# Optimization experiments

Measured on AMD Instinct MI355X. Metric: run time of the kernel, lower is better.

Reference implementation:

```python
import jax, jax.numpy as jnp
import numpy as np

LEAKY_ALPHA = 0.2

def setup_inputs() -> dict:
    key = jax.random.key(0)
    kA, kH, kW, k1, k2 = jax.random.split(key, 5)
    B, N, F_in, D = 8, 2048, 256, 128
    return {
        "A": jax.random.normal(kA, (B, N, N), dtype=jnp.float32),
        "H": jax.random.normal(kH, (B, N, F_in), dtype=jnp.float32),
        "W": jax.random.normal(kW, (F_in, D), dtype=jnp.float32) * 0.05,
        "a_1": jax.random.normal(k1, (D, 1), dtype=jnp.float32) * 0.05,
        "a_2": jax.random.normal(k2, (D, 1), dtype=jnp.float32) * 0.05,
    }

def reference(A, H, W, a_1, a_2):
    # H_: [B, N, D] node projections
    H_ = jnp.einsum('bnf,fd->bnd', H, W)
    # additive attention logits: f1[b,i] + f2[b,j] -> [B, N, N]
    f1 = H_ @ a_1            # [B, N, 1]
    f2 = H_ @ a_2            # [B, N, 1]
    e = jax.nn.leaky_relu(f1 + jnp.swapaxes(f2, 1, 2), negative_slope=LEAKY_ALPHA)
    # NOTE: original multiplies logits by the binary adjacency (not -inf masking)
    mask = (A > 0.0).astype(jnp.float32)
    alpha = jax.nn.softmax(e * mask, axis=-1)   # [B, N, N]
    H_next = jnp.matmul(alpha, H_)              # [B, N, D]
    return H_next
```

## Files before the change

kernel.cpp:

```cpp
#include <hip/hip_runtime.h>


#define LEAKY 0.2f
constexpr int Bb = 8, Nn = 2048, FIN = 256, Dd = 128;
constexpr int NROW = Bb * Nn;

typedef __attribute__((ext_vector_type(8))) short short8;
typedef __attribute__((ext_vector_type(4))) float float4v;

__device__ __forceinline__ unsigned short f2bf(float f) {
    union { float f; unsigned int i; } v; v.f = f;
    return (unsigned short)((v.i + 0x8000u) >> 16);
}

__global__ __launch_bounds__(256) void prep_wt(const float* __restrict__ W,
                                               unsigned short* __restrict__ Wt) {
    int idx = blockIdx.x * 256 + threadIdx.x;
    int k = idx >> 7, d = idx & 127;
    Wt[d * FIN + k] = f2bf(W[idx]);
}

__global__ __launch_bounds__(256) void proj_kernel(
    const float* __restrict__ Hg,
    const unsigned short* __restrict__ Wt,
    const float* __restrict__ a1, const float* __restrict__ a2,
    unsigned short* __restrict__ Hbt,
    float* __restrict__ f1g, float* __restrict__ f2g) {
    constexpr int WS = 264;
    __shared__ unsigned short Wl[128 * WS];
    __shared__ float Fb[2][2][2][16];
    const int tid = threadIdx.x;

    #pragma unroll
    for (int p = 0; p < 16; ++p) {
        int i8 = p * 2048 + tid * 8;
        int n = i8 >> 8, k = i8 & 255;
        *(uint4*)(Wl + n * WS + k) = *(const uint4*)(Wt + i8);
    }
    __syncthreads();

    const int wave = tid >> 6, lane = tid & 63;
    const int r = wave >> 1, h = wave & 1;
    const int q = lane >> 4, m = lane & 15;
    const int row0 = blockIdx.x * 32 + 16 * r;
    const float* hrow = Hg + (size_t)(row0 + m) * FIN;

    float4v acc[4] = {};
    #pragma unroll 2
    for (int c = 0; c < 8; ++c) {
        float4 ha = *(const float4*)(hrow + 32 * c + 8 * q);
        float4 hb = *(const float4*)(hrow + 32 * c + 8 * q + 4);
        union { short8 v; unsigned int u[4]; } A;
        A.u[0] = (unsigned)f2bf(ha.x) | ((unsigned)f2bf(ha.y) << 16);
        A.u[1] = (unsigned)f2bf(ha.z) | ((unsigned)f2bf(ha.w) << 16);
        A.u[2] = (unsigned)f2bf(hb.x) | ((unsigned)f2bf(hb.y) << 16);
        A.u[3] = (unsigned)f2bf(hb.z) | ((unsigned)f2bf(hb.w) << 16);
        #pragma unroll
        for (int t = 0; t < 4; ++t) {
            int n = 64 * h + 16 * t + m;
            short8 bfr = *(const short8*)(Wl + n * WS + 32 * c + 8 * q);
            acc[t] = __builtin_amdgcn_mfma_f32_16x16x32_bf16(A.v, bfr, acc[t], 0, 0, 0);
        }
    }
    float p1[4] = {0.f, 0.f, 0.f, 0.f}, p2[4] = {0.f, 0.f, 0.f, 0.f};
    #pragma unroll
    for (int t = 0; t < 4; ++t) {
        int n = 64 * h + 16 * t + m;
        ushort4 hv;
        hv.x = f2bf(acc[t][0]); hv.y = f2bf(acc[t][1]);
        hv.z = f2bf(acc[t][2]); hv.w = f2bf(acc[t][3]);
        *(ushort4*)(Hbt + (size_t)n * NROW + row0 + 4 * q) = hv;
        float w1 = a1[n], w2 = a2[n];
        #pragma unroll
        for (int rg = 0; rg < 4; ++rg) {
            p1[rg] = fmaf(acc[t][rg], w1, p1[rg]);
            p2[rg] = fmaf(acc[t][rg], w2, p2[rg]);
        }
    }
    #pragma unroll
    for (int off = 1; off <= 8; off <<= 1) {
        #pragma unroll
        for (int rg = 0; rg < 4; ++rg) {
            p1[rg] += __shfl_xor(p1[rg], off, 64);
            p2[rg] += __shfl_xor(p2[rg], off, 64);
        }
    }
    if (m == 0) {
        #pragma unroll
        for (int rg = 0; rg < 4; ++rg) {
            Fb[0][r][h][4 * q + rg] = p1[rg];
            Fb[1][r][h][4 * q + rg] = p2[rg];
        }
    }
    __syncthreads();
    if (tid < 32) {
        int r2 = tid >> 4, i = tid & 15;
        int row = blockIdx.x * 32 + 16 * r2 + i;
        f1g[row] = Fb[0][r2][0][i] + Fb[0][r2][1][i];
        f2g[row] = Fb[1][r2][0][i] + Fb[1][r2][1][i];
    }
}

__global__ __launch_bounds__(256) void attn_kernel(
    const float* __restrict__ Ag,
    const unsigned short* __restrict__ Hbt,
    const float* __restrict__ f1g, const float* __restrict__ f2g,
    float* __restrict__ Og) {
    constexpr int RS = 132;
    __shared__ float Rbuf[4 * 16 * RS];
    __shared__ float Lbuf[4][16];

    const int tid = threadIdx.x;
    const int w = tid >> 6, lane = tid & 63;
    const int q = lane >> 4, m = lane & 15;
    const int b = blockIdx.y;
    const int i0 = blockIdx.x * 16;
    const size_t bRow = (size_t)b * Nn;

    const float fi = f1g[bRow + i0 + m];
    const float* Arow = Ag + (bRow + i0 + m) * (size_t)Nn;
    const float* f2p = f2g + bRow;
    const unsigned short* Bbase = Hbt + (size_t)m * NROW + bRow;

    float4v acc[8] = {};
    float lsum = 0.f;
    const int j0 = w * (Nn / 4);

    #pragma unroll 2
    for (int jt = j0; jt < j0 + Nn / 4; jt += 64) {
        short8 pa[2];
        #pragma unroll
        for (int c = 0; c < 2; ++c) {
            int col = jt + 32 * c + 8 * q;
            float4 a0 = *(const float4*)(Arow + col);
            float4 a1v = *(const float4*)(Arow + col + 4);
            float4 fa = *(const float4*)(f2p + col);
            float4 fb = *(const float4*)(f2p + col + 4);
            float av[8] = {a0.x, a0.y, a0.z, a0.w, a1v.x, a1v.y, a1v.z, a1v.w};
            float fv[8] = {fa.x, fa.y, fa.z, fa.w, fb.x, fb.y, fb.z, fb.w};
            union { short8 v; unsigned short us[8]; } P;
            #pragma unroll
            for (int j = 0; j < 8; ++j) {
                float s = fi + fv[j];
                float e = fmaxf(s, LEAKY * s);
                e = fminf(e, 30.f);
                float p = (av[j] > 0.f) ? __expf(e) : 1.0f;
                P.us[j] = f2bf(p);
                lsum += p;
            }
            pa[c] = P.v;
        }
        #pragma unroll
        for (int t = 0; t < 8; ++t) {
            const unsigned short* bp = Bbase + (size_t)(16 * t) * NROW + jt + 8 * q;
            short8 b0 = *(const short8*)(bp);
            short8 b1 = *(const short8*)(bp + 32);
            acc[t] = __builtin_amdgcn_mfma_f32_16x16x32_bf16(pa[0], b0, acc[t], 0, 0, 0);
            acc[t] = __builtin_amdgcn_mfma_f32_16x16x32_bf16(pa[1], b1, acc[t], 0, 0, 0);
        }
    }

    lsum += __shfl_xor(lsum, 16, 64);
    lsum += __shfl_xor(lsum, 32, 64);
    if (lane < 16) Lbuf[w][lane] = lsum;
    #pragma unroll
    for (int t = 0; t < 8; ++t)
        #pragma unroll
        for (int rg = 0; rg < 4; ++rg)
            Rbuf[w * 16 * RS + (4 * q + rg) * RS + 16 * t + m] = acc[t][rg];
    __syncthreads();

    const int row = tid >> 4, c4 = tid & 15;
    float l = Lbuf[0][row] + Lbuf[1][row] + Lbuf[2][row] + Lbuf[3][row];
    float rl = 1.0f / l;
    float* orow = Og + (bRow + i0 + row) * (size_t)Dd;
    #pragma unroll
    for (int half = 0; half < 2; ++half) {
        int col = 64 * half + 4 * c4;
        const float* rb = Rbuf + row * RS + col;
        float4 s0 = *(const float4*)(rb);
        float4 s1 = *(const float4*)(rb + 16 * RS);
        float4 s2 = *(const float4*)(rb + 32 * RS);
        float4 s3 = *(const float4*)(rb + 48 * RS);
        float4 o;
        o.x = (s0.x + s1.x + s2.x + s3.x) * rl;
        o.y = (s0.y + s1.y + s2.y + s3.y) * rl;
        o.z = (s0.z + s1.z + s2.z + s3.z) * rl;
        o.w = (s0.w + s1.w + s2.w + s3.w) * rl;
        *(float4*)(orow + col) = o;
    }
}

extern "C" void kernel_launch(void* const* d_in, const int* in_sizes, int n_in,
                              void* d_out, int out_size, void* d_ws, size_t ws_size,
                              hipStream_t stream) {
    const float* A  = (const float*)d_in[0];
    const float* H  = (const float*)d_in[1];
    const float* W  = (const float*)d_in[2];
    const float* a1 = (const float*)d_in[3];
    const float* a2 = (const float*)d_in[4];
    float* out = (float*)d_out;

    unsigned short* Wt  = (unsigned short*)d_ws;
    unsigned short* Hbt = Wt + FIN * Dd;
    float* f1 = (float*)(Hbt + (size_t)Dd * NROW);
    float* f2 = f1 + NROW;

    prep_wt<<<dim3(FIN * Dd / 256), 256, 0, stream>>>(W, Wt);
    proj_kernel<<<dim3(NROW / 32), 256, 0, stream>>>(H, Wt, a1, a2, Hbt, f1, f2);
    attn_kernel<<<dim3(Nn / 16, Bb), 256, 0, stream>>>(A, Hbt, f1, f2, out);
}
```

Measured before the change: 259.8 us.

## Software-pipeline A/f2 loads in attention and drop LDS staging in projection

```diff
diff --git a/kernel.cpp b/kernel.cpp
--- a/kernel.cpp
+++ b/kernel.cpp
@@ -20,52 +20,48 @@
     Wt[d * FIN + k] = f2bf(W[idx]);
 }
 
-__global__ __launch_bounds__(256) void proj_kernel(
+__global__ __launch_bounds__(128) void proj_kernel(
     const float* __restrict__ Hg,
     const unsigned short* __restrict__ Wt,
     const float* __restrict__ a1, const float* __restrict__ a2,
     unsigned short* __restrict__ Hbt,
     float* __restrict__ f1g, float* __restrict__ f2g) {
-    constexpr int WS = 264;
-    __shared__ unsigned short Wl[128 * WS];
-    __shared__ float Fb[2][2][2][16];
     const int tid = threadIdx.x;
-
-    #pragma unroll
-    for (int p = 0; p < 16; ++p) {
-        int i8 = p * 2048 + tid * 8;
-        int n = i8 >> 8, k = i8 & 255;
-        *(uint4*)(Wl + n * WS + k) = *(const uint4*)(Wt + i8);
-    }
-    __syncthreads();
-
     const int wave = tid >> 6, lane = tid & 63;
-    const int r = wave >> 1, h = wave & 1;
     const int q = lane >> 4, m = lane & 15;
-    const int row0 = blockIdx.x * 32 + 16 * r;
+    const int row0 = blockIdx.x * 32 + 16 * wave;
     const float* hrow = Hg + (size_t)(row0 + m) * FIN;
 
-    float4v acc[4] = {};
-    #pragma unroll 2
+    float4v acc[8] = {};
+    float4 Ab0 = *(const float4*)(hrow + 8 * q);
+    float4 Ab1 = *(const float4*)(hrow + 8 * q + 4);
+
+    #pragma unroll
     for (int c = 0; c < 8; ++c) {
-        float4 ha = *(const float4*)(hrow + 32 * c + 8 * q);
-        float4 hb = *(const float4*)(hrow + 32 * c + 8 * q + 4);
         union { short8 v; unsigned int u[4]; } A;
-        A.u[0] = (unsigned)f2bf(ha.x) | ((unsigned)f2bf(ha.y) << 16);
-        A.u[1] = (unsigned)f2bf(ha.z) | ((unsigned)f2bf(ha.w) << 16);
-        A.u[2] = (unsigned)f2bf(hb.x) | ((unsigned)f2bf(hb.y) << 16);
-        A.u[3] = (unsigned)f2bf(hb.z) | ((unsigned)f2bf(hb.w) << 16);
-        #pragma unroll
-        for (int t = 0; t < 4; ++t) {
-            int n = 64 * h + 16 * t + m;
-            short8 bfr = *(const short8*)(Wl + n * WS + 32 * c + 8 * q);
-            acc[t] = __builtin_amdgcn_mfma_f32_16x16x32_bf16(A.v, bfr, acc[t], 0, 0, 0);
-        }
-    }
+        A.u[0] = (unsigned)f2bf(Ab0.x) | ((unsigned)f2bf(Ab0.y) << 16);
+        A.u[1] = (unsigned)f2bf(Ab0.z) | ((unsigned)f2bf(Ab0.w) << 16);
+        A.u[2] = (unsigned)f2bf(Ab1.x) | ((unsigned)f2bf(Ab1.y) << 16);
+        A.u[3] = (unsigned)f2bf(Ab1.z) | ((unsigned)f2bf(Ab1.w) << 16);
+        short8 bf[8];
+        #pragma unroll
+        for (int t = 0; t < 8; ++t)
+            bf[t] = *(const short8*)(Wt + (size_t)(16 * t + m) * FIN + 32 * c + 8 * q);
+        __builtin_amdgcn_sched_barrier(0);
+        if (c < 7) {
+            Ab0 = *(const float4*)(hrow + 32 * (c + 1) + 8 * q);
+            Ab1 = *(const float4*)(hrow + 32 * (c + 1) + 8 * q + 4);
+        }
+        __builtin_amdgcn_sched_barrier(0);
+        #pragma unroll
+        for (int t = 0; t < 8; ++t)
+            acc[t] = __builtin_amdgcn_mfma_f32_16x16x32_bf16(A.v, bf[t], acc[t], 0, 0, 0);
+    }
+
     float p1[4] = {0.f, 0.f, 0.f, 0.f}, p2[4] = {0.f, 0.f, 0.f, 0.f};
     #pragma unroll
-    for (int t = 0; t < 4; ++t) {
-        int n = 64 * h + 16 * t + m;
+    for (int t = 0; t < 8; ++t) {
+        int n = 16 * t + m;
         ushort4 hv;
         hv.x = f2bf(acc[t][0]); hv.y = f2bf(acc[t][1]);
         hv.z = f2bf(acc[t][2]); hv.w = f2bf(acc[t][3]);
@@ -88,16 +84,9 @@
     if (m == 0) {
         #pragma unroll
         for (int rg = 0; rg < 4; ++rg) {
-            Fb[0][r][h][4 * q + rg] = p1[rg];
-            Fb[1][r][h][4 * q + rg] = p2[rg];
-        }
-    }
-    __syncthreads();
-    if (tid < 32) {
-        int r2 = tid >> 4, i = tid & 15;
-        int row = blockIdx.x * 32 + 16 * r2 + i;
-        f1g[row] = Fb[0][r2][0][i] + Fb[0][r2][1][i];
-        f2g[row] = Fb[1][r2][0][i] + Fb[1][r2][1][i];
+            f1g[row0 + 4 * q + rg] = p1[rg];
+            f2g[row0 + 4 * q + rg] = p2[rg];
+        }
     }
 }
 
@@ -125,19 +114,26 @@
     float4v acc[8] = {};
     float lsum = 0.f;
     const int j0 = w * (Nn / 4);
-
-    #pragma unroll 2
-    for (int jt = j0; jt < j0 + Nn / 4; jt += 64) {
+    const int jend = j0 + Nn / 4;
+
+    float4 Ab[4], Fb[4];
+    Ab[0] = *(const float4*)(Arow + j0 + 8 * q);
+    Ab[1] = *(const float4*)(Arow + j0 + 8 * q + 4);
+    Ab[2] = *(const float4*)(Arow + j0 + 32 + 8 * q);
+    Ab[3] = *(const float4*)(Arow + j0 + 32 + 8 * q + 4);
+    Fb[0] = *(const float4*)(f2p + j0 + 8 * q);
+    Fb[1] = *(const float4*)(f2p + j0 + 8 * q + 4);
+    Fb[2] = *(const float4*)(f2p + j0 + 32 + 8 * q);
+    Fb[3] = *(const float4*)(f2p + j0 + 32 + 8 * q + 4);
+
+    for (int jt = j0; jt < jend; jt += 64) {
         short8 pa[2];
         #pragma unroll
         for (int c = 0; c < 2; ++c) {
-            int col = jt + 32 * c + 8 * q;
-            float4 a0 = *(const float4*)(Arow + col);
-            float4 a1v = *(const float4*)(Arow + col + 4);
-            float4 fa = *(const float4*)(f2p + col);
-            float4 fb = *(const float4*)(f2p + col + 4);
-            float av[8] = {a0.x, a0.y, a0.z, a0.w, a1v.x, a1v.y, a1v.z, a1v.w};
-            float fv[8] = {fa.x, fa.y, fa.z, fa.w, fb.x, fb.y, fb.z, fb.w};
+            float av[8] = {Ab[2*c].x, Ab[2*c].y, Ab[2*c].z, Ab[2*c].w,
+                           Ab[2*c+1].x, Ab[2*c+1].y, Ab[2*c+1].z, Ab[2*c+1].w};
+            float fv[8] = {Fb[2*c].x, Fb[2*c].y, Fb[2*c].z, Fb[2*c].w,
+                           Fb[2*c+1].x, Fb[2*c+1].y, Fb[2*c+1].z, Fb[2*c+1].w};
             union { short8 v; unsigned short us[8]; } P;
             #pragma unroll
             for (int j = 0; j < 8; ++j) {
@@ -150,13 +146,31 @@
             }
             pa[c] = P.v;
         }
+        short8 bf[16];
         #pragma unroll
         for (int t = 0; t < 8; ++t) {
             const unsigned short* bp = Bbase + (size_t)(16 * t) * NROW + jt + 8 * q;
-            short8 b0 = *(const short8*)(bp);
-            short8 b1 = *(const short8*)(bp + 32);
-            acc[t] = __builtin_amdgcn_mfma_f32_16x16x32_bf16(pa[0], b0, acc[t], 0, 0, 0);
-            acc[t] = __builtin_amdgcn_mfma_f32_16x16x32_bf16(pa[1], b1, acc[t], 0, 0, 0);
+            bf[2 * t]     = *(const short8*)(bp);
+            bf[2 * t + 1] = *(const short8*)(bp + 32);
+        }
+        __builtin_amdgcn_sched_barrier(0);
+        if (jt + 64 < jend) {
+            const float* ar = Arow + jt + 64;
+            Ab[0] = *(const float4*)(ar + 8 * q);
+            Ab[1] = *(const float4*)(ar + 8 * q + 4);
+            Ab[2] = *(const float4*)(ar + 32 + 8 * q);
+            Ab[3] = *(const float4*)(ar + 32 + 8 * q + 4);
+            const float* fr = f2p + jt + 64;
+            Fb[0] = *(const float4*)(fr + 8 * q);
+            Fb[1] = *(const float4*)(fr + 8 * q + 4);
+            Fb[2] = *(const float4*)(fr + 32 + 8 * q);
+            Fb[3] = *(const float4*)(fr + 32 + 8 * q + 4);
+        }
+        __builtin_amdgcn_sched_barrier(0);
+        #pragma unroll
+        for (int t = 0; t < 8; ++t) {
+            acc[t] = __builtin_amdgcn_mfma_f32_16x16x32_bf16(pa[0], bf[2*t],     acc[t], 0, 0, 0);
+            acc[t] = __builtin_amdgcn_mfma_f32_16x16x32_bf16(pa[1], bf[2*t + 1], acc[t], 0, 0, 0);
         }
     }
 
@@ -207,6 +221,6 @@
     float* f2 = f1 + NROW;
 
     prep_wt<<<dim3(FIN * Dd / 256), 256, 0, stream>>>(W, Wt);
-    proj_kernel<<<dim3(NROW / 32), 256, 0, stream>>>(H, Wt, a1, a2, Hbt, f1, f2);
+    proj_kernel<<<dim3(NROW / 32), 128, 0, stream>>>(H, Wt, a1, a2, Hbt, f1, f2);
     attn_kernel<<<dim3(Nn / 16, Bb), 256, 0, stream>>>(A, Hbt, f1, f2, out);
 }
```

New measurement: 253.7 us. -2.3%, faster.

## Stage A tiles through double-buffered LDS and pack H and W in MFMA fragment layout

Applied to the files above, without the earlier changes.

```diff
diff --git a/kernel.cpp b/kernel.cpp
--- a/kernel.cpp
+++ b/kernel.cpp
@@ -4,6 +4,7 @@
 #define LEAKY 0.2f
 constexpr int Bb = 8, Nn = 2048, FIN = 256, Dd = 128;
 constexpr int NROW = Bb * Nn;
+constexpr int RS = 132;
 
 typedef __attribute__((ext_vector_type(8))) short short8;
 typedef __attribute__((ext_vector_type(4))) float float4v;
@@ -13,138 +14,173 @@
     return (unsigned short)((v.i + 0x8000u) >> 16);
 }
 
-__global__ __launch_bounds__(256) void prep_wt(const float* __restrict__ W,
-                                               unsigned short* __restrict__ Wt) {
+__device__ __forceinline__ void stage_read(const float* __restrict__ base, int rstride,
+                                           int tid, float4* st) {
+    const int row = tid >> 4, c16 = tid & 15;
+    const float* p = base + (size_t)row * rstride + c16 * 4;
+    #pragma unroll
+    for (int k = 0; k < 4; ++k) st[k] = *(const float4*)(p + 64 * k);
+}
+__device__ __forceinline__ void stage_write(float* __restrict__ As, int tid, const float4* st) {
+    const int row = tid >> 4, c16 = tid & 15, sw = row & 7;
+    float* dst = As + row * 256;
+    #pragma unroll
+    for (int k = 0; k < 4; ++k) {
+        const int col = 4 * (c16 + 16 * k);
+        dst[(col + 0) ^ sw] = st[k].x;
+        dst[(col + 1) ^ sw] = st[k].y;
+        dst[(col + 2) ^ sw] = st[k].z;
+        dst[(col + 3) ^ sw] = st[k].w;
+    }
+}
+
+__global__ __launch_bounds__(256) void prep_wf(const float* __restrict__ W,
+                                               unsigned short* __restrict__ Wf) {
     int idx = blockIdx.x * 256 + threadIdx.x;
     int k = idx >> 7, d = idx & 127;
-    Wt[d * FIN + k] = f2bf(W[idx]);
+    Wf[(size_t)((k >> 3) * 128 + d) * 8 + (k & 7)] = f2bf(W[idx]);
 }
 
 __global__ __launch_bounds__(256) void proj_kernel(
     const float* __restrict__ Hg,
-    const unsigned short* __restrict__ Wt,
+    const unsigned short* __restrict__ Wf,
     const float* __restrict__ a1, const float* __restrict__ a2,
-    unsigned short* __restrict__ Hbt,
+    unsigned short* __restrict__ Hbt2,
     float* __restrict__ f1g, float* __restrict__ f2g) {
-    constexpr int WS = 264;
-    __shared__ unsigned short Wl[128 * WS];
-    __shared__ float Fb[2][2][2][16];
+    __shared__ float Rbuf[4 * 16 * RS];
+    __shared__ float Hs[4096];
+
     const int tid = threadIdx.x;
-
-    #pragma unroll
-    for (int p = 0; p < 16; ++p) {
-        int i8 = p * 2048 + tid * 8;
-        int n = i8 >> 8, k = i8 & 255;
-        *(uint4*)(Wl + n * WS + k) = *(const uint4*)(Wt + i8);
-    }
-    __syncthreads();
-
-    const int wave = tid >> 6, lane = tid & 63;
-    const int r = wave >> 1, h = wave & 1;
-    const int q = lane >> 4, m = lane & 15;
-    const int row0 = blockIdx.x * 32 + 16 * r;
-    const float* hrow = Hg + (size_t)(row0 + m) * FIN;
-
-    float4v acc[4] = {};
-    #pragma unroll 2
-    for (int c = 0; c < 8; ++c) {
-        float4 ha = *(const float4*)(hrow + 32 * c + 8 * q);
-        float4 hb = *(const float4*)(hrow + 32 * c + 8 * q + 4);
-        union { short8 v; unsigned int u[4]; } A;
-        A.u[0] = (unsigned)f2bf(ha.x) | ((unsigned)f2bf(ha.y) << 16);
-        A.u[1] = (unsigned)f2bf(ha.z) | ((unsigned)f2bf(ha.w) << 16);
-        A.u[2] = (unsigned)f2bf(hb.x) | ((unsigned)f2bf(hb.y) << 16);
-        A.u[3] = (unsigned)f2bf(hb.z) | ((unsigned)f2bf(hb.w) << 16);
-        #pragma unroll
-        for (int t = 0; t < 4; ++t) {
-            int n = 64 * h + 16 * t + m;
-            short8 bfr = *(const short8*)(Wl + n * WS + 32 * c + 8 * q);
-            acc[t] = __builtin_amdgcn_mfma_f32_16x16x32_bf16(A.v, bfr, acc[t], 0, 0, 0);
-        }
-    }
-    float p1[4] = {0.f, 0.f, 0.f, 0.f}, p2[4] = {0.f, 0.f, 0.f, 0.f};
-    #pragma unroll
-    for (int t = 0; t < 4; ++t) {
-        int n = 64 * h + 16 * t + m;
-        ushort4 hv;
-        hv.x = f2bf(acc[t][0]); hv.y = f2bf(acc[t][1]);
-        hv.z = f2bf(acc[t][2]); hv.w = f2bf(acc[t][3]);
-        *(ushort4*)(Hbt + (size_t)n * NROW + row0 + 4 * q) = hv;
-        float w1 = a1[n], w2 = a2[n];
-        #pragma unroll
-        for (int rg = 0; rg < 4; ++rg) {
-            p1[rg] = fmaf(acc[t][rg], w1, p1[rg]);
-            p2[rg] = fmaf(acc[t][rg], w2, p2[rg]);
-        }
-    }
-    #pragma unroll
-    for (int off = 1; off <= 8; off <<= 1) {
-        #pragma unroll
-        for (int rg = 0; rg < 4; ++rg) {
-            p1[rg] += __shfl_xor(p1[rg], off, 64);
-            p2[rg] += __shfl_xor(p2[rg], off, 64);
-        }
-    }
-    if (m == 0) {
-        #pragma unroll
-        for (int rg = 0; rg < 4; ++rg) {
-            Fb[0][r][h][4 * q + rg] = p1[rg];
-            Fb[1][r][h][4 * q + rg] = p2[rg];
-        }
-    }
-    __syncthreads();
-    if (tid < 32) {
-        int r2 = tid >> 4, i = tid & 15;
-        int row = blockIdx.x * 32 + 16 * r2 + i;
-        f1g[row] = Fb[0][r2][0][i] + Fb[0][r2][1][i];
-        f2g[row] = Fb[1][r2][0][i] + Fb[1][r2][1][i];
-    }
+    const int w = tid >> 6, lane = tid & 63, q = lane >> 4, m = lane & 15;
+    const int row0 = blockIdx.x * 16;
+
+    float4 st[4];
+    stage_read(Hg + (size_t)row0 * FIN, FIN, tid, st);
+    stage_write(Hs, tid, st);
+    __syncthreads();
+
+    float4v acc[8] = {};
+    const float* arow = Hs + m * 256;
+    const int sw = m & 7;
+    #pragma unroll
+    for (int c = 0; c < 2; ++c) {
+        const int cb = w * 64 + 32 * c + 8 * q;
+        union { short8 v; unsigned short us[8]; } Af;
+        #pragma unroll
+        for (int j = 0; j < 8; ++j) Af.us[j] = f2bf(arow[cb + (j ^ sw)]);
+        #pragma unroll
+        for (int t = 0; t < 8; ++t) {
+            const short8 bfr = *(const short8*)(Wf + (size_t)((8 * w + 4 * c + q) * 128 + 16 * t + m) * 8);
+            acc[t] = __builtin_amdgcn_mfma_f32_16x16x32_bf16(Af.v, bfr, acc[t], 0, 0, 0);
+        }
+    }
+    #pragma unroll
+    for (int t = 0; t < 8; ++t)
+        #pragma unroll
+        for (int rg = 0; rg < 4; ++rg)
+            Rbuf[w * 16 * RS + (4 * q + rg) * RS + 16 * t + m] = acc[t][rg];
+    __syncthreads();
+
+    const int row = tid >> 4, c4 = tid & 15;
+    float o[8];
+    #pragma unroll
+    for (int half = 0; half < 2; ++half) {
+        const int col = 64 * half + 4 * c4;
+        const float* rb = Rbuf + row * RS + col;
+        float4 s0 = *(const float4*)(rb);
+        float4 s1 = *(const float4*)(rb + 16 * RS);
+        float4 s2 = *(const float4*)(rb + 32 * RS);
+        float4 s3 = *(const float4*)(rb + 48 * RS);
+        o[4 * half + 0] = s0.x + s1.x + s2.x + s3.x;
+        o[4 * half + 1] = s0.y + s1.y + s2.y + s3.y;
+        o[4 * half + 2] = s0.z + s1.z + s2.z + s3.z;
+        o[4 * half + 3] = s0.w + s1.w + s2.w + s3.w;
+    }
+    {
+        float4 A1a = *(const float4*)(a1 + 4 * c4), A1b = *(const float4*)(a1 + 64 + 4 * c4);
+        float4 A2a = *(const float4*)(a2 + 4 * c4), A2b = *(const float4*)(a2 + 64 + 4 * c4);
+        float p1 = o[0]*A1a.x + o[1]*A1a.y + o[2]*A1a.z + o[3]*A1a.w
+                 + o[4]*A1b.x + o[5]*A1b.y + o[6]*A1b.z + o[7]*A1b.w;
+        float p2 = o[0]*A2a.x + o[1]*A2a.y + o[2]*A2a.z + o[3]*A2a.w
+                 + o[4]*A2b.x + o[5]*A2b.y + o[6]*A2b.z + o[7]*A2b.w;
+        #pragma unroll
+        for (int off = 1; off <= 8; off <<= 1) {
+            p1 += __shfl_xor(p1, off, 16);
+            p2 += __shfl_xor(p2, off, 16);
+        }
+        if (c4 == 0) { f1g[row0 + row] = p1; f2g[row0 + row] = p2; }
+    }
+    *(float4*)(Rbuf + row * RS + 4 * c4)      = make_float4(o[0], o[1], o[2], o[3]);
+    *(float4*)(Rbuf + row * RS + 64 + 4 * c4) = make_float4(o[4], o[5], o[6], o[7]);
+    __syncthreads();
+    const int d = tid >> 1, h = tid & 1;
+    union { uint4 v; unsigned short us[8]; } oP;
+    #pragma unroll
+    for (int r = 0; r < 8; ++r) oP.us[r] = f2bf(Rbuf[(8 * h + r) * RS + d]);
+    *(uint4*)(Hbt2 + (size_t)((2 * blockIdx.x + h) * 128 + d) * 8) = oP.v;
 }
 
 __global__ __launch_bounds__(256) void attn_kernel(
     const float* __restrict__ Ag,
-    const unsigned short* __restrict__ Hbt,
+    const unsigned short* __restrict__ Hbt2,
     const float* __restrict__ f1g, const float* __restrict__ f2g,
     float* __restrict__ Og) {
-    constexpr int RS = 132;
-    __shared__ float Rbuf[4 * 16 * RS];
+    __shared__ float smem[8448];
+    __shared__ float f2s[2][256];
     __shared__ float Lbuf[4][16];
 
     const int tid = threadIdx.x;
-    const int w = tid >> 6, lane = tid & 63;
-    const int q = lane >> 4, m = lane & 15;
-    const int b = blockIdx.y;
-    const int i0 = blockIdx.x * 16;
+    const int w = tid >> 6, lane = tid & 63, q = lane >> 4, m = lane & 15;
+    const int b = blockIdx.y, i0 = blockIdx.x * 16;
     const size_t bRow = (size_t)b * Nn;
 
     const float fi = f1g[bRow + i0 + m];
-    const float* Arow = Ag + (bRow + i0 + m) * (size_t)Nn;
+    const float* Abase = Ag + (bRow + i0) * (size_t)Nn;
     const float* f2p = f2g + bRow;
-    const unsigned short* Bbase = Hbt + (size_t)m * NROW + bRow;
+    const unsigned short* Bb2 = Hbt2 + bRow * 128;
+    const int jw = w * 64;
 
     float4v acc[8] = {};
     float lsum = 0.f;
-    const int j0 = w * (Nn / 4);
-
-    #pragma unroll 2
-    for (int jt = j0; jt < j0 + Nn / 4; jt += 64) {
+    float4 st[4], fst;
+
+    stage_read(Abase, Nn, tid, st);
+    if (tid < 64) fst = *(const float4*)(f2p + tid * 4);
+    stage_write(smem, tid, st);
+    if (tid < 64) *(float4*)(&f2s[0][tid * 4]) = fst;
+
+    for (int ch = 0; ch < 8; ++ch) {
+        __syncthreads();
+        const int jt = ch * 256;
+        const float* As = smem + (ch & 1) * 4096;
+        const float* f2c = &f2s[ch & 1][0];
+        const unsigned short* bg = Bb2 + (size_t)((jt + jw) >> 3) * 1024;
+        short8 bf[16];
+        #pragma unroll
+        for (int t = 0; t < 8; ++t) {
+            bf[2 * t]     = *(const short8*)(bg + ((size_t)(q    ) * 128 + 16 * t + m) * 8);
+            bf[2 * t + 1] = *(const short8*)(bg + ((size_t)(q + 4) * 128 + 16 * t + m) * 8);
+        }
+        __builtin_amdgcn_sched_barrier(0);
+        if (ch < 7) {
+            stage_read(Abase + jt + 256, Nn, tid, st);
+            if (tid < 64) fst = *(const float4*)(f2p + jt + 256 + tid * 4);
+        }
+        __builtin_amdgcn_sched_barrier(0);
+        const float* arow = As + m * 256;
+        const int sw = m & 7;
         short8 pa[2];
         #pragma unroll
         for (int c = 0; c < 2; ++c) {
-            int col = jt + 32 * c + 8 * q;
-            float4 a0 = *(const float4*)(Arow + col);
-            float4 a1v = *(const float4*)(Arow + col + 4);
-            float4 fa = *(const float4*)(f2p + col);
-            float4 fb = *(const float4*)(f2p + col + 4);
-            float av[8] = {a0.x, a0.y, a0.z, a0.w, a1v.x, a1v.y, a1v.z, a1v.w};
-            float fv[8] = {fa.x, fa.y, fa.z, fa.w, fb.x, fb.y, fb.z, fb.w};
+            const int cb = jw + 32 * c + 8 * q;
             union { short8 v; unsigned short us[8]; } P;
             #pragma unroll
             for (int j = 0; j < 8; ++j) {
-                float s = fi + fv[j];
+                const float a = arow[cb + (j ^ sw)];
+                const float s = fi + f2c[cb + j];
                 float e = fmaxf(s, LEAKY * s);
                 e = fminf(e, 30.f);
-                float p = (av[j] > 0.f) ? __expf(e) : 1.0f;
+                const float p = (a > 0.f) ? __expf(e) : 1.0f;
                 P.us[j] = f2bf(p);
                 lsum += p;
             }
@@ -152,17 +188,20 @@
         }
         #pragma unroll
         for (int t = 0; t < 8; ++t) {
-            const unsigned short* bp = Bbase + (size_t)(16 * t) * NROW + jt + 8 * q;
-            short8 b0 = *(const short8*)(bp);
-            short8 b1 = *(const short8*)(bp + 32);
-            acc[t] = __builtin_amdgcn_mfma_f32_16x16x32_bf16(pa[0], b0, acc[t], 0, 0, 0);
-            acc[t] = __builtin_amdgcn_mfma_f32_16x16x32_bf16(pa[1], b1, acc[t], 0, 0, 0);
-        }
-    }
-
+            acc[t] = __builtin_amdgcn_mfma_f32_16x16x32_bf16(pa[0], bf[2 * t],     acc[t], 0, 0, 0);
+            acc[t] = __builtin_amdgcn_mfma_f32_16x16x32_bf16(pa[1], bf[2 * t + 1], acc[t], 0, 0, 0);
+        }
+        if (ch < 7) {
+            stage_write(smem + ((ch + 1) & 1) * 4096, tid, st);
+            if (tid < 64) *(float4*)(&f2s[(ch + 1) & 1][tid * 4]) = fst;
+        }
+    }
+
+    __syncthreads();
     lsum += __shfl_xor(lsum, 16, 64);
     lsum += __shfl_xor(lsum, 32, 64);
     if (lane < 16) Lbuf[w][lane] = lsum;
+    float* Rbuf = smem;
     #pragma unroll
     for (int t = 0; t < 8; ++t)
         #pragma unroll
@@ -176,7 +215,7 @@
     float* orow = Og + (bRow + i0 + row) * (size_t)Dd;
     #pragma unroll
     for (int half = 0; half < 2; ++half) {
-        int col = 64 * half + 4 * c4;
+        const int col = 64 * half + 4 * c4;
         const float* rb = Rbuf + row * RS + col;
         float4 s0 = *(const float4*)(rb);
         float4 s1 = *(const float4*)(rb + 16 * RS);
@@ -201,12 +240,12 @@
     const float* a2 = (const float*)d_in[4];
     float* out = (float*)d_out;
 
-    unsigned short* Wt  = (unsigned short*)d_ws;
-    unsigned short* Hbt = Wt + FIN * Dd;
-    float* f1 = (float*)(Hbt + (size_t)Dd * NROW);
+    unsigned short* Wf   = (unsigned short*)d_ws;
+    unsigned short* Hbt2 = Wf + FIN * Dd;
+    float* f1 = (float*)(Hbt2 + (size_t)Dd * NROW);
     float* f2 = f1 + NROW;
 
-    prep_wt<<<dim3(FIN * Dd / 256), 256, 0, stream>>>(W, Wt);
-    proj_kernel<<<dim3(NROW / 32), 256, 0, stream>>>(H, Wt, a1, a2, Hbt, f1, f2);
-    attn_kernel<<<dim3(Nn / 16, Bb), 256, 0, stream>>>(A, Hbt, f1, f2, out);
-}
+    prep_wf<<<dim3(FIN * Dd / 256), 256, 0, stream>>>(W, Wf);
+    proj_kernel<<<dim3(NROW / 16), 256, 0, stream>>>(H, Wf, a1, a2, Hbt2, f1, f2);
+    attn_kernel<<<dim3(Nn / 16, Bb), 256, 0, stream>>>(A, Hbt2, f1, f2, out);
+}
```

After: 224.2 us. -13.7%, faster.
